# Kernel optimization log

Measured on AMD Instinct MI355X. Metric: run time of the kernel, lower is better.

The kernel has to match this reference:

```python
import jax, jax.numpy as jnp
import numpy as np


def setup_inputs() -> dict:
    key = jax.random.key(0)
    k1, _ = jax.random.split(key)
    B, H, W, C = 8, 128, 128, 512
    inputs = jax.random.normal(k1, (B, H, W, C), dtype=jnp.float32)
    gamma = jnp.ones((), dtype=jnp.float32)
    return {"inputs": inputs, "gamma": gamma}


def reference(inputs, gamma):
    B, H, W, C = inputs.shape
    q = inputs.reshape(B, H * W, C).astype(jnp.float32)  # [B, HW, C]
    # attention = key @ query = q^T q  -> [B, C, C]
    attn = jnp.einsum('bnc,bnd->bcd', q, q)
    # reversed-softmax trick: softmax(max - attn) over last axis
    attn = jnp.max(attn, axis=-1, keepdims=True) - attn
    attn = jax.nn.softmax(attn, axis=-1)
    # value = query @ attention -> [B, HW, C]
    value = jnp.einsum('bnc,bcd->bnd', q, attn)
    value = value.astype(inputs.dtype).reshape(B, H, W, C)
    return gamma * value + inputs
```

## Files before the change

### kernel.cpp

```cpp
#include <hip/hip_runtime.h>
#include <hip/hip_bf16.h>

#define B_  8
#define C_  512
#define NN  16384
#define SPL 8
#define KB_ (NN / SPL)
#define TT  (KB_ / 64)

typedef _Float16 half8 __attribute__((ext_vector_type(8)));
typedef float    f32x4 __attribute__((ext_vector_type(4)));

__device__ __forceinline__ unsigned short f2h(float x) {
    union { _Float16 h; unsigned short u; } cv;
    cv.h = (_Float16)x;
    return cv.u;
}

__device__ __forceinline__ void gload16(const unsigned short* src, unsigned short* ldst) {
    __builtin_amdgcn_global_load_lds(
        (const __attribute__((address_space(1))) void*)src,
        (__attribute__((address_space(3))) void*)ldst,
        16, 0, 0);
}

__global__ void ws_probe_kernel(float* out, float v) { out[0] = v; }

__global__ __launch_bounds__(256) void pack_kernel(const float* __restrict__ in,
                                                   unsigned short* __restrict__ qT,
                                                   unsigned short* __restrict__ qn) {
    __shared__ unsigned short lh[64][72];
    int t  = threadIdx.x;
    int n0 = blockIdx.x * 64;
    int c0 = blockIdx.y * 64;
    int b  = blockIdx.z;
    const float* ib = in + ((size_t)b * NN + n0) * C_ + c0;
#pragma unroll
    for (int p = 0; p < 4; ++p) {
        int nl = p * 16 + (t >> 4);
        int cl = (t & 15) * 4;
        float4 v = *(const float4*)(ib + (size_t)nl * C_ + cl);
        ushort4 q4;
        q4.x = f2h(v.x); q4.y = f2h(v.y); q4.z = f2h(v.z); q4.w = f2h(v.w);
        lh[cl + 0][nl] = q4.x;
        lh[cl + 1][nl] = q4.y;
        lh[cl + 2][nl] = q4.z;
        lh[cl + 3][nl] = q4.w;
        *(ushort4*)(qn + ((size_t)b * NN + n0 + nl) * C_ + c0 + cl) = q4;
    }
    __syncthreads();
    size_t obase = ((size_t)b * C_ + c0) * NN + n0;
#pragma unroll
    for (int p = 0; p < 2; ++p) {
        int cr = p * 32 + (t >> 3);
        int nf = (t & 7) * 8;
        *(uint4*)(qT + obase + (size_t)cr * NN + nf) = *(const uint4*)&lh[cr][nf];
    }
}

__global__ __launch_bounds__(512, 2) void gram_kernel(const unsigned short* __restrict__ qT,
                                                      float* __restrict__ P) {
    __shared__ unsigned short sA[2][16384];
    __shared__ unsigned short sB[2][16384];
    int t = threadIdx.x, lane = t & 63, wave = t >> 6;
    int wr = wave >> 2, wc = wave & 3;
    int bid = blockIdx.x;
    int b = bid & 7, r = bid >> 3;
    int tile = r & 3, split = r >> 2;
    int tc = tile >> 1, td = tile & 1;
    size_t qb = (size_t)b * C_ * NN;
    const unsigned short* Ap = qT + qb + (size_t)(tc * 256) * NN + (size_t)split * KB_;
    const unsigned short* Bp = qT + qb + (size_t)(td * 256) * NN + (size_t)split * KB_;

    f32x4 acc[8][4];
#pragma unroll
    for (int m = 0; m < 8; ++m)
#pragma unroll
        for (int n = 0; n < 4; ++n) acc[m][n] = (f32x4){0.f, 0.f, 0.f, 0.f};

    int o0 = t * 16,         u0 = o0 ^ (((o0 >> 9) & 1) << 5);
    int o1 = (t + 512) * 16, u1 = o1 ^ (((o1 >> 9) & 1) << 5);
    int rih0 = u0 >> 7, k0 = (u0 & 127) >> 1;
    int rih1 = u1 >> 7, k1 = (u1 & 127) >> 1;

#define STAGE(dst, dd, h, panel, kt)                                                        \
    do {                                                                                    \
        gload16((panel) + (size_t)((h)*128 + rih0) * NN + (kt)*64 + k0,                     \
                &dst[dd][(h)*8192 + t * 8]);                                                \
        gload16((panel) + (size_t)((h)*128 + rih1) * NN + (kt)*64 + k1,                     \
                &dst[dd][(h)*8192 + (t + 512) * 8]);                                        \
    } while (0)

    int g16 = (lane >> 4) * 16;
#define AFRAG(dd, row, ks) \
    (*(const half8*)((const char*)&sA[dd][0] + (((row)*128 + (ks)*64 + g16) ^ (((row)&4) << 3))))
#define BFRAG(dd, row, ks) \
    (*(const half8*)((const char*)&sB[dd][0] + (((row)*128 + (ks)*64 + g16) ^ (((row)&4) << 3))))

    STAGE(sA, 0, 0, Ap, 0);
    STAGE(sB, 0, 0, Bp, 0);
    STAGE(sB, 0, 1, Bp, 0);
    STAGE(sA, 0, 1, Ap, 0);
    asm volatile("s_waitcnt vmcnt(2)" ::: "memory");
    __builtin_amdgcn_s_barrier();

    for (int kt = 0; kt < TT; ++kt) {
        int d = kt & 1, nd = d ^ 1;
        half8 aF[4][2], b0F[2][2], b1F[2][2];
#pragma unroll
        for (int m = 0; m < 4; ++m) {
            int row = wr * 64 + m * 16 + (lane & 15);
#pragma unroll
            for (int ks = 0; ks < 2; ++ks) aF[m][ks] = AFRAG(d, row, ks);
        }
#pragma unroll
        for (int n = 0; n < 2; ++n) {
            int row0 = wc * 32 + n * 16 + (lane & 15);
#pragma unroll
            for (int ks = 0; ks < 2; ++ks) {
                b0F[n][ks] = BFRAG(d, row0, ks);
                b1F[n][ks] = BFRAG(d, (row0 + 128), ks);
            }
        }
        if (kt + 1 < TT) {
            STAGE(sA, nd, 0, Ap, kt + 1);
            STAGE(sB, nd, 0, Bp, kt + 1);
            STAGE(sB, nd, 1, Bp, kt + 1);
        }
        __builtin_amdgcn_s_setprio(1);
#pragma unroll
        for (int m = 0; m < 4; ++m)
#pragma unroll
            for (int n = 0; n < 2; ++n)
#pragma unroll
                for (int ks = 0; ks < 2; ++ks) {
                    acc[m][n]     = __builtin_amdgcn_mfma_f32_16x16x32_f16(aF[m][ks], b0F[n][ks], acc[m][n],     0, 0, 0);
                    acc[m][n + 2] = __builtin_amdgcn_mfma_f32_16x16x32_f16(aF[m][ks], b1F[n][ks], acc[m][n + 2], 0, 0, 0);
                }
        __builtin_amdgcn_s_setprio(0);
        if (kt + 1 < TT) {
            asm volatile("s_waitcnt vmcnt(6)" ::: "memory");
        } else {
            asm volatile("s_waitcnt vmcnt(0)" ::: "memory");
        }
        __builtin_amdgcn_s_barrier();
#pragma unroll
        for (int m = 0; m < 4; ++m) {
            int row = 128 + wr * 64 + m * 16 + (lane & 15);
#pragma unroll
            for (int ks = 0; ks < 2; ++ks) aF[m][ks] = AFRAG(d, row, ks);
        }
        if (kt + 1 < TT) STAGE(sA, nd, 1, Ap, kt + 1);
        __builtin_amdgcn_s_setprio(1);
#pragma unroll
        for (int m = 0; m < 4; ++m)
#pragma unroll
            for (int n = 0; n < 2; ++n)
#pragma unroll
                for (int ks = 0; ks < 2; ++ks) {
                    acc[m + 4][n + 2] = __builtin_amdgcn_mfma_f32_16x16x32_f16(aF[m][ks], b1F[n][ks], acc[m + 4][n + 2], 0, 0, 0);
                    acc[m + 4][n]     = __builtin_amdgcn_mfma_f32_16x16x32_f16(aF[m][ks], b0F[n][ks], acc[m + 4][n],     0, 0, 0);
                }
        __builtin_amdgcn_s_setprio(0);
        asm volatile("s_waitcnt vmcnt(2)" ::: "memory");
        __builtin_amdgcn_s_barrier();
    }

    float* outp = P + ((size_t)(split * 8 + b)) * (C_ * C_);
#pragma unroll
    for (int m = 0; m < 8; ++m) {
        int row0 = tc * 256 + wr * 64 + (m & 3) * 16 + (m >> 2) * 128 + (lane >> 4) * 4;
#pragma unroll
        for (int n = 0; n < 4; ++n) {
            int col = td * 256 + wc * 32 + (n & 1) * 16 + (n >> 1) * 128 + (lane & 15);
#pragma unroll
            for (int j = 0; j < 4; ++j)
                outp[(size_t)(row0 + j) * C_ + col] = acc[m][n][j];
        }
    }
#undef STAGE
#undef AFRAG
#undef BFRAG
}

__global__ __launch_bounds__(256) void softmax_kernel(const float* __restrict__ P,
                                                      unsigned short* __restrict__ WT) {
    __shared__ unsigned short lw[C_ * 4];
    int t = threadIdx.x, lane = t & 63, wave = t >> 6;
    int b = blockIdx.y;
    int c = blockIdx.x * 4 + wave;
    const float* base = P + (size_t)b * (C_ * C_) + (size_t)c * C_;

    float g[8];
    float mn = 3.4e38f;
#pragma unroll
    for (int k = 0; k < 8; ++k) {
        int d = k * 64 + lane;
        float v = 0.f;
#pragma unroll
        for (int s = 0; s < 8; ++s) v += base[(size_t)s * (8 * C_ * C_) + d];
        g[k] = v;
        mn = fminf(mn, v);
    }
#pragma unroll
    for (int o = 32; o; o >>= 1) mn = fminf(mn, __shfl_xor(mn, o));
    float w[8];
    float sum = 0.f;
#pragma unroll
    for (int k = 0; k < 8; ++k) { w[k] = __expf(mn - g[k]); sum += w[k]; }
#pragma unroll
    for (int o = 32; o; o >>= 1) sum += __shfl_xor(sum, o);
    float inv = 1.0f / sum;
#pragma unroll
    for (int k = 0; k < 8; ++k) {
        int d = k * 64 + lane;
        lw[d * 4 + wave] = f2h(w[k] * inv);
    }
    __syncthreads();
    int c0 = blockIdx.x * 4;
    for (int d = t; d < C_; d += 256)
        *(ushort4*)(WT + ((size_t)b * C_ + d) * C_ + c0) = *(ushort4*)&lw[d * 4];
}

__global__ __launch_bounds__(512, 2) void value_kernel(const unsigned short* __restrict__ qn,
                                                       const unsigned short* __restrict__ WT,
                                                       const float* __restrict__ gamma,
                                                       float* __restrict__ out) {
    __shared__ unsigned short sA[2][16384];
    __shared__ unsigned short sB[2][16384];
    int t = threadIdx.x, lane = t & 63, wave = t >> 6;
    int wr = wave >> 2, wc = wave & 3;
    int bid = blockIdx.x;
    int b = bid & 7, r = bid >> 3;
    int dt = r & 1, nt = r >> 1;
    const unsigned short* Ap = qn + ((size_t)b * NN + (size_t)nt * 256) * C_;
    const unsigned short* Bp = WT + ((size_t)b * C_ + dt * 256) * C_;

    f32x4 acc[8][4];
#pragma unroll
    for (int m = 0; m < 8; ++m)
#pragma unroll
        for (int n = 0; n < 4; ++n) acc[m][n] = (f32x4){0.f, 0.f, 0.f, 0.f};

    int o0 = t * 16,         u0 = o0 ^ (((o0 >> 9) & 1) << 5);
    int o1 = (t + 512) * 16, u1 = o1 ^ (((o1 >> 9) & 1) << 5);
    int rih0 = u0 >> 7, k0 = (u0 & 127) >> 1;
    int rih1 = u1 >> 7, k1 = (u1 & 127) >> 1;

#define STAGE(dst, dd, h, panel, kt)                                                        \
    do {                                                                                    \
        gload16((panel) + (size_t)((h)*128 + rih0) * C_ + (kt)*64 + k0,                     \
                &dst[dd][(h)*8192 + t * 8]);                                                \
        gload16((panel) + (size_t)((h)*128 + rih1) * C_ + (kt)*64 + k1,                     \
                &dst[dd][(h)*8192 + (t + 512) * 8]);                                        \
    } while (0)

    int g16 = (lane >> 4) * 16;
#define AFRAG(dd, row, ks) \
    (*(const half8*)((const char*)&sA[dd][0] + (((row)*128 + (ks)*64 + g16) ^ (((row)&4) << 3))))
#define BFRAG(dd, row, ks) \
    (*(const half8*)((const char*)&sB[dd][0] + (((row)*128 + (ks)*64 + g16) ^ (((row)&4) << 3))))

    STAGE(sA, 0, 0, Ap, 0);
    STAGE(sB, 0, 0, Bp, 0);
    STAGE(sB, 0, 1, Bp, 0);
    STAGE(sA, 0, 1, Ap, 0);
    asm volatile("s_waitcnt vmcnt(2)" ::: "memory");
    __builtin_amdgcn_s_barrier();

    for (int kt = 0; kt < 8; ++kt) {
        int d = kt & 1, nd = d ^ 1;
        half8 aF[4][2], b0F[2][2], b1F[2][2];
#pragma unroll
        for (int m = 0; m < 4; ++m) {
            int row = wr * 64 + m * 16 + (lane & 15);
#pragma unroll
            for (int ks = 0; ks < 2; ++ks) aF[m][ks] = AFRAG(d, row, ks);
        }
#pragma unroll
        for (int n = 0; n < 2; ++n) {
            int row0 = wc * 32 + n * 16 + (lane & 15);
#pragma unroll
            for (int ks = 0; ks < 2; ++ks) {
                b0F[n][ks] = BFRAG(d, row0, ks);
                b1F[n][ks] = BFRAG(d, (row0 + 128), ks);
            }
        }
        if (kt + 1 < 8) {
            STAGE(sA, nd, 0, Ap, kt + 1);
            STAGE(sB, nd, 0, Bp, kt + 1);
            STAGE(sB, nd, 1, Bp, kt + 1);
        }
        __builtin_amdgcn_s_setprio(1);
#pragma unroll
        for (int m = 0; m < 4; ++m)
#pragma unroll
            for (int n = 0; n < 2; ++n)
#pragma unroll
                for (int ks = 0; ks < 2; ++ks) {
                    acc[m][n]     = __builtin_amdgcn_mfma_f32_16x16x32_f16(aF[m][ks], b0F[n][ks], acc[m][n],     0, 0, 0);
                    acc[m][n + 2] = __builtin_amdgcn_mfma_f32_16x16x32_f16(aF[m][ks], b1F[n][ks], acc[m][n + 2], 0, 0, 0);
                }
        __builtin_amdgcn_s_setprio(0);
        if (kt + 1 < 8) {
            asm volatile("s_waitcnt vmcnt(6)" ::: "memory");
        } else {
            asm volatile("s_waitcnt vmcnt(0)" ::: "memory");
        }
        __builtin_amdgcn_s_barrier();
#pragma unroll
        for (int m = 0; m < 4; ++m) {
            int row = 128 + wr * 64 + m * 16 + (lane & 15);
#pragma unroll
            for (int ks = 0; ks < 2; ++ks) aF[m][ks] = AFRAG(d, row, ks);
        }
        if (kt + 1 < 8) STAGE(sA, nd, 1, Ap, kt + 1);
        __builtin_amdgcn_s_setprio(1);
#pragma unroll
        for (int m = 0; m < 4; ++m)
#pragma unroll
            for (int n = 0; n < 2; ++n)
#pragma unroll
                for (int ks = 0; ks < 2; ++ks) {
                    acc[m + 4][n + 2] = __builtin_amdgcn_mfma_f32_16x16x32_f16(aF[m][ks], b1F[n][ks], acc[m + 4][n + 2], 0, 0, 0);
                    acc[m + 4][n]     = __builtin_amdgcn_mfma_f32_16x16x32_f16(aF[m][ks], b0F[n][ks], acc[m + 4][n],     0, 0, 0);
                }
        __builtin_amdgcn_s_setprio(0);
        asm volatile("s_waitcnt vmcnt(2)" ::: "memory");
        __builtin_amdgcn_s_barrier();
    }

    float gm = gamma[0];
#pragma unroll
    for (int m = 0; m < 8; ++m) {
        int row0 = nt * 256 + wr * 64 + (m & 3) * 16 + (m >> 2) * 128 + (lane >> 4) * 4;
#pragma unroll
        for (int n = 0; n < 4; ++n) {
            int col = dt * 256 + wc * 32 + (n & 1) * 16 + (n >> 1) * 128 + (lane & 15);
#pragma unroll
            for (int j = 0; j < 4; ++j) {
                size_t idx = ((size_t)b * NN + (row0 + j)) * C_ + col;
                float iv = (float)(*(const _Float16*)&qn[idx]);
                out[idx] = gm * acc[m][n][j] + iv;
            }
        }
    }
#undef STAGE
#undef AFRAG
#undef BFRAG
}

extern "C" void kernel_launch(void* const* d_in, const int* in_sizes, int n_in,
                              void* d_out, int out_size, void* d_ws, size_t ws_size,
                              hipStream_t stream) {
    const float* in    = (const float*)d_in[0];
    const float* gamma = (const float*)d_in[1];
    float* out = (float*)d_out;

    const size_t q_elems = (size_t)B_ * C_ * NN;
    const size_t p_elems = (size_t)B_ * C_ * C_;
    const size_t need = q_elems * 2
                      + q_elems * 2
                      + (size_t)SPL * p_elems * 4
                      + p_elems * 2;
    if (ws_size < need) {
        ws_probe_kernel<<<1, 1, 0, stream>>>(out, (float)ws_size);
        return;
    }

    unsigned short* qT = (unsigned short*)d_ws;
    unsigned short* qn = qT + q_elems;
    float* P = (float*)(qn + q_elems);
    unsigned short* WT = (unsigned short*)(P + (size_t)SPL * p_elems);

    pack_kernel<<<dim3(NN / 64, C_ / 64, B_), 256, 0, stream>>>(in, qT, qn);
    gram_kernel<<<256, 512, 0, stream>>>(qT, P);
    softmax_kernel<<<dim3(C_ / 4, B_), 256, 0, stream>>>(P, WT);
    value_kernel<<<1024, 512, 0, stream>>>(qn, WT, gamma, out);
}
```

Before: 339.7 us.

## Make value kernel persistent over four row tiles with overlapped epilogue

The value kernel now launches 256 blocks, each walking four consecutive 256-row tiles in one continuous 32-step pipeline instead of 1024 blocks each doing one tile. The next tile's loads are issued around the epilogue stores so prologue and tail costs are amortised and loads overlap the output writes. The B panel is still re-streamed for each tile. Fewer blocks (256 on a large GPU at 2 blocks/CU) may underfill the device, and the epilogue stays serialised inside the loop.

Result: slower. 563.4 us (+65.9%).

```diff
diff --git a/kernel.cpp b/kernel.cpp
--- a/kernel.cpp
+++ b/kernel.cpp
@@ -232,9 +232,10 @@
     int wr = wave >> 2, wc = wave & 3;
     int bid = blockIdx.x;
     int b = bid & 7, r = bid >> 3;
-    int dt = r & 1, nt = r >> 1;
-    const unsigned short* Ap = qn + ((size_t)b * NN + (size_t)nt * 256) * C_;
-    const unsigned short* Bp = WT + ((size_t)b * C_ + dt * 256) * C_;
+    int dt = r & 1, ntg = r >> 1;
+    const unsigned short* Ap0 = qn + ((size_t)b * NN + (size_t)ntg * 1024) * C_;
+    const unsigned short* Bp  = WT + ((size_t)b * C_ + dt * 256) * C_;
+    float gm = gamma[0];
 
     f32x4 acc[8][4];
 #pragma unroll
@@ -247,49 +248,56 @@
     int rih0 = u0 >> 7, k0 = (u0 & 127) >> 1;
     int rih1 = u1 >> 7, k1 = (u1 & 127) >> 1;
 
-#define STAGE(dst, dd, h, panel, kt)                                                        \
+#define STAGEV(dst, dd, h, apanel, col)                                                     \
     do {                                                                                    \
-        gload16((panel) + (size_t)((h)*128 + rih0) * C_ + (kt)*64 + k0,                     \
+        gload16((apanel) + (size_t)((h)*128 + rih0) * C_ + (col) + k0,                      \
                 &dst[dd][(h)*8192 + t * 8]);                                                \
-        gload16((panel) + (size_t)((h)*128 + rih1) * C_ + (kt)*64 + k1,                     \
+        gload16((apanel) + (size_t)((h)*128 + rih1) * C_ + (col) + k1,                      \
                 &dst[dd][(h)*8192 + (t + 512) * 8]);                                        \
     } while (0)
 
     int g16 = (lane >> 4) * 16;
+    int l15 = lane & 15;
 #define AFRAG(dd, row, ks) \
     (*(const half8*)((const char*)&sA[dd][0] + (((row)*128 + (ks)*64 + g16) ^ (((row)&4) << 3))))
 #define BFRAG(dd, row, ks) \
     (*(const half8*)((const char*)&sB[dd][0] + (((row)*128 + (ks)*64 + g16) ^ (((row)&4) << 3))))
 
-    STAGE(sA, 0, 0, Ap, 0);
-    STAGE(sB, 0, 0, Bp, 0);
-    STAGE(sB, 0, 1, Bp, 0);
-    STAGE(sA, 0, 1, Ap, 0);
+    STAGEV(sA, 0, 0, Ap0, 0);
+    STAGEV(sB, 0, 0, Bp, 0);
+    STAGEV(sB, 0, 1, Bp, 0);
+    STAGEV(sA, 0, 1, Ap0, 0);
     asm volatile("s_waitcnt vmcnt(2)" ::: "memory");
     __builtin_amdgcn_s_barrier();
 
-    for (int kt = 0; kt < 8; ++kt) {
-        int d = kt & 1, nd = d ^ 1;
+#pragma unroll 1
+    for (int s = 0; s < 32; ++s) {
+        int d = s & 1, nd = d ^ 1;
+        const unsigned short* An = Ap0 + (size_t)((s + 1) >> 3) * 256 * C_;
+        int coln = ((s + 1) & 7) * 64;
+        bool last = (s == 31);
+        bool epi  = ((s & 7) == 7);
+
         half8 aF[4][2], b0F[2][2], b1F[2][2];
 #pragma unroll
         for (int m = 0; m < 4; ++m) {
-            int row = wr * 64 + m * 16 + (lane & 15);
+            int row = wr * 64 + m * 16 + l15;
 #pragma unroll
             for (int ks = 0; ks < 2; ++ks) aF[m][ks] = AFRAG(d, row, ks);
         }
 #pragma unroll
         for (int n = 0; n < 2; ++n) {
-            int row0 = wc * 32 + n * 16 + (lane & 15);
+            int row0 = wc * 32 + n * 16 + l15;
 #pragma unroll
             for (int ks = 0; ks < 2; ++ks) {
                 b0F[n][ks] = BFRAG(d, row0, ks);
                 b1F[n][ks] = BFRAG(d, (row0 + 128), ks);
             }
         }
-        if (kt + 1 < 8) {
-            STAGE(sA, nd, 0, Ap, kt + 1);
-            STAGE(sB, nd, 0, Bp, kt + 1);
-            STAGE(sB, nd, 1, Bp, kt + 1);
+        if (!last) {
+            STAGEV(sA, nd, 0, An, coln);
+            STAGEV(sB, nd, 0, Bp, coln);
+            STAGEV(sB, nd, 1, Bp, coln);
         }
         __builtin_amdgcn_s_setprio(1);
 #pragma unroll
@@ -302,19 +310,20 @@
                     acc[m][n + 2] = __builtin_amdgcn_mfma_f32_16x16x32_f16(aF[m][ks], b1F[n][ks], acc[m][n + 2], 0, 0, 0);
                 }
         __builtin_amdgcn_s_setprio(0);
-        if (kt + 1 < 8) {
+        if (!last) {
             asm volatile("s_waitcnt vmcnt(6)" ::: "memory");
         } else {
             asm volatile("s_waitcnt vmcnt(0)" ::: "memory");
         }
         __builtin_amdgcn_s_barrier();
+
 #pragma unroll
         for (int m = 0; m < 4; ++m) {
-            int row = 128 + wr * 64 + m * 16 + (lane & 15);
+            int row = 128 + wr * 64 + m * 16 + l15;
 #pragma unroll
             for (int ks = 0; ks < 2; ++ks) aF[m][ks] = AFRAG(d, row, ks);
         }
-        if (kt + 1 < 8) STAGE(sA, nd, 1, Ap, kt + 1);
+        if (!epi && !last) STAGEV(sA, nd, 1, An, coln);
         __builtin_amdgcn_s_setprio(1);
 #pragma unroll
         for (int m = 0; m < 4; ++m)
@@ -326,26 +335,33 @@
                     acc[m + 4][n]     = __builtin_amdgcn_mfma_f32_16x16x32_f16(aF[m][ks], b0F[n][ks], acc[m + 4][n],     0, 0, 0);
                 }
         __builtin_amdgcn_s_setprio(0);
-        asm volatile("s_waitcnt vmcnt(2)" ::: "memory");
-        __builtin_amdgcn_s_barrier();
-    }
-
-    float gm = gamma[0];
-#pragma unroll
-    for (int m = 0; m < 8; ++m) {
-        int row0 = nt * 256 + wr * 64 + (m & 3) * 16 + (m >> 2) * 128 + (lane >> 4) * 4;
-#pragma unroll
-        for (int n = 0; n < 4; ++n) {
-            int col = dt * 256 + wc * 32 + (n & 1) * 16 + (n >> 1) * 128 + (lane & 15);
-#pragma unroll
-            for (int j = 0; j < 4; ++j) {
-                size_t idx = ((size_t)b * NN + (row0 + j)) * C_ + col;
-                float iv = (float)(*(const _Float16*)&qn[idx]);
-                out[idx] = gm * acc[m][n][j] + iv;
+
+        if (epi) {
+            int nrow_base = (ntg * 4 + (s >> 3)) * 256;
+#pragma unroll
+            for (int m = 0; m < 8; ++m) {
+                int row0 = nrow_base + wr * 64 + (m & 3) * 16 + (m >> 2) * 128 + (lane >> 4) * 4;
+#pragma unroll
+                for (int n = 0; n < 4; ++n) {
+                    int col = dt * 256 + wc * 32 + (n & 1) * 16 + (n >> 1) * 128 + l15;
+#pragma unroll
+                    for (int j = 0; j < 4; ++j) {
+                        size_t idx = ((size_t)b * NN + (row0 + j)) * C_ + col;
+                        float iv = (float)(*(const _Float16*)&qn[idx]);
+                        out[idx] = gm * acc[m][n][j] + iv;
+                        acc[m][n][j] = 0.f;
+                    }
+                }
             }
-        }
-    }
-#undef STAGE
+            if (!last) STAGEV(sA, nd, 1, An, coln);
+        }
+
+        if (!last) {
+            asm volatile("s_waitcnt vmcnt(2)" ::: "memory");
+            __builtin_amdgcn_s_barrier();
+        }
+    }
+#undef STAGEV
 #undef AFRAG
 #undef BFRAG
 }
@@ -376,5 +392,5 @@
     pack_kernel<<<dim3(NN / 64, C_ / 64, B_), 256, 0, stream>>>(in, qT, qn);
     gram_kernel<<<256, 512, 0, stream>>>(qT, P);
     softmax_kernel<<<dim3(C_ / 4, B_), 256, 0, stream>>>(P, WT);
-    value_kernel<<<1024, 512, 0, stream>>>(qn, WT, gamma, out);
-}
+    value_kernel<<<256, 512, 0, stream>>>(qn, WT, gamma, out);
+}
```
